# Kernel tuning notes

Measured on AMD Instinct MI355X. Metric: run time of the kernel, lower is better.

## Reference

```python
import jax, jax.numpy as jnp
import numpy as np

N = 2048      # feature_num (nodes/sensors)
T = 5         # timd_num (window length)
D = 64        # embed_dim
TOPK = 21     # topk + 1 (includes self, cos(i,i)=1)
B = 32        # batch
EPS = 1e-5
NEG_SLOPE = 0.2


def setup_inputs() -> dict:
    key = jax.random.key(0)
    ks = jax.random.split(key, 9)
    s = 1.0 / np.sqrt(D)
    return {
        "x": jax.random.normal(ks[0], (B, N, T), jnp.float32),
        "emb": jax.random.normal(ks[1], (N, D), jnp.float32) * s,      # embedding table
        "W": jax.random.normal(ks[2], (D, T), jnp.float32) * (1.0 / np.sqrt(T)),  # GNN lin weight
        "Wb": jax.random.normal(ks[3], (D,), jnp.float32) * 0.01,       # GNN lin bias
        "a_src": jax.random.normal(ks[4], (2 * D,), jnp.float32) * s,   # attention vec (source half)
        "a_dst": jax.random.normal(ks[5], (2 * D,), jnp.float32) * s,   # attention vec (dest half)
        "gamma": jnp.ones((D,), jnp.float32),                            # BatchNorm1d weight
        "beta": jnp.zeros((D,), jnp.float32),                            # BatchNorm1d bias
        "fc_w": jax.random.normal(ks[6], (1, D), jnp.float32) * s,      # fc weight
        "fc_b": jnp.zeros((1,), jnp.float32),                            # fc bias
    }


def reference(x, emb, W, Wb, a_src, a_dst, gamma, beta, fc_w, fc_b):
    # --- cosine-sim topk graph build ---
    norm = jnp.linalg.norm(emb, axis=-1)                    # [N]
    cos = (emb @ emb.T) / (norm[:, None] * norm[None, :])   # [N,N]
    _, idx = jax.lax.top_k(cos, TOPK)                       # [N,TOPK]
    # scatter one-hot adjacency (vectorized, no per-row loop)
    adj = jnp.zeros((N, N), x.dtype).at[jnp.arange(N)[:, None], idx].set(1.0)
    # --- GNN: GDN-style attention message passing ---
    h = jnp.einsum('bnt,dt->bnd', x, W) + Wb                # [B,N,D]
    g = jnp.concatenate([h, jnp.broadcast_to(emb, h.shape)], axis=-1)  # [B,N,2D]
    e_src = g @ a_src                                       # [B,N]
    e_dst = g @ a_dst                                       # [B,N]
    e = jax.nn.leaky_relu(e_src[:, :, None] + e_dst[:, None, :], NEG_SLOPE)  # [B,N,N]
    e = jnp.where(adj > 0, e, jnp.float32(-1e9))
    alpha = jax.nn.softmax(e, axis=-1)                      # [B,N,N], rows sum to 1 over TOPK nbrs
    z = jax.nn.relu(jnp.einsum('bij,bjd->bid', alpha, h))   # [B,N,D]
    # --- output head: z * emb, BN over channels, relu, fc ---
    out = z * emb                                           # [B,N,D]
    mean = out.mean(axis=(0, 1))                            # BN1d stats over (batch, nodes)
    var = out.var(axis=(0, 1))
    out = (out - mean) * jax.lax.rsqrt(var + EPS) * gamma + beta
    out = jax.nn.relu(out)
    out = out @ fc_w.T + fc_b                               # [B,N,1]
    return out.reshape(-1, N)                               # [B,N]
```

## Files before the change

### kernel.cpp

```cpp
#include <hip/hip_runtime.h>
#include <math.h>

#define N_NODES 2048
#define T_WIN 5
#define D_EMB 64
#define TOPK 21
#define B_BATCH 32
#define BN_TOTAL (B_BATCH * N_NODES)
#define EPS_BN 1e-5f
#define NEG_SLOPE 0.2f
#define STATS_STRIDE 16

typedef unsigned long long u64;

__device__ __forceinline__ float wave_sum(float v) {
#pragma unroll
    for (int off = 32; off > 0; off >>= 1) v += __shfl_xor(v, off, 64);
    return v;
}

__device__ __forceinline__ u64 max64(u64 a, u64 b) { return a > b ? a : b; }
__device__ __forceinline__ u64 min64(u64 a, u64 b) { return a < b ? a : b; }

__device__ __forceinline__ u64 bitonic_sort64_desc(u64 key, int lane) {
#pragma unroll
    for (int k = 2; k <= 64; k <<= 1) {
#pragma unroll
        for (int j = k >> 1; j >= 1; j >>= 1) {
            u64 pk = __shfl_xor(key, j, 64);
            bool dirDesc = ((lane & k) == 0);
            bool keepMax = (((lane & j) == 0) == dirDesc);
            key = keepMax ? max64(key, pk) : min64(key, pk);
        }
    }
    return key;
}

__device__ __forceinline__ u64 bitonic_merge_top64(u64 a, u64 b, int lane) {
    u64 br = __shfl(b, 63 - lane, 64);
    u64 c = max64(a, br);
#pragma unroll
    for (int j = 32; j >= 1; j >>= 1) {
        u64 pk = __shfl_xor(c, j, 64);
        bool keepMax = ((lane & j) == 0);
        c = keepMax ? max64(c, pk) : min64(c, pk);
    }
    return c;
}

__global__ __launch_bounds__(64) void k_node_pre(
    const float* __restrict__ emb, float* __restrict__ norms,
    float* __restrict__ stats, float* __restrict__ stats2) {
    int n = blockIdx.x;
    int d = threadIdx.x;
    if (n < 16) stats[n * 64 + d] = 0.f;
    else if (n < 32) stats2[(n - 16) * 64 + d] = 0.f;
    float e = emb[n * D_EMB + d];
    float s2 = wave_sum(e * e);
    if (d == 0) norms[n] = sqrtf(s2);
}

__global__ __launch_bounds__(256) void k_gram(
    const float* __restrict__ emb, const float* __restrict__ norms,
    float* __restrict__ cosM) {
    __shared__ __align__(16) float As[64][68];
    __shared__ __align__(16) float Bs[64][68];
    int t = threadIdx.x;
    int bi = blockIdx.x & 31, bj = blockIdx.x >> 5;
    int i0 = bi * 64, j0 = bj * 64;

    {
        int r = t >> 2, c0 = t & 3;
        const float4* srcA = (const float4*)(emb + (size_t)(i0 + r) * D_EMB);
        const float4* srcB = (const float4*)(emb + (size_t)(j0 + r) * D_EMB);
#pragma unroll
        for (int k = 0; k < 4; k++) {
            int f4 = c0 + 4 * k;
            float4 v = srcA[f4];
            int d = 4 * f4;
            As[d][r] = v.x; As[d + 1][r] = v.y; As[d + 2][r] = v.z; As[d + 3][r] = v.w;
            float4 w = srcB[f4];
            Bs[d][r] = w.x; Bs[d + 1][r] = w.y; Bs[d + 2][r] = w.z; Bs[d + 3][r] = w.w;
        }
    }
    __syncthreads();

    int ti = t & 15, tj = t >> 4;
    float acc[4][4] = {};
#pragma unroll
    for (int d = 0; d < 64; d++) {
        float4 a = *(const float4*)&As[d][4 * ti];
        float4 b = *(const float4*)&Bs[d][4 * tj];
        acc[0][0] += a.x * b.x; acc[0][1] += a.x * b.y; acc[0][2] += a.x * b.z; acc[0][3] += a.x * b.w;
        acc[1][0] += a.y * b.x; acc[1][1] += a.y * b.y; acc[1][2] += a.y * b.z; acc[1][3] += a.y * b.w;
        acc[2][0] += a.z * b.x; acc[2][1] += a.z * b.y; acc[2][2] += a.z * b.z; acc[2][3] += a.z * b.w;
        acc[3][0] += a.w * b.x; acc[3][1] += a.w * b.y; acc[3][2] += a.w * b.z; acc[3][3] += a.w * b.w;
    }

    float nis[4] = {norms[i0 + 4 * ti], norms[i0 + 4 * ti + 1],
                    norms[i0 + 4 * ti + 2], norms[i0 + 4 * ti + 3]};
    float njs[4] = {norms[j0 + 4 * tj], norms[j0 + 4 * tj + 1],
                    norms[j0 + 4 * tj + 2], norms[j0 + 4 * tj + 3]};
#pragma unroll
    for (int r = 0; r < 4; r++) {
        float4 o;
        o.x = acc[r][0] / (nis[r] * njs[0]);
        o.y = acc[r][1] / (nis[r] * njs[1]);
        o.z = acc[r][2] / (nis[r] * njs[2]);
        o.w = acc[r][3] / (nis[r] * njs[3]);
        *(float4*)(cosM + (size_t)(i0 + 4 * ti + r) * N_NODES + j0 + 4 * tj) = o;
    }
}

__global__ __launch_bounds__(256) void k_select(
    const float* __restrict__ cosM, int* __restrict__ idxT) {
    __shared__ u64 candbuf[4][128];
    int tid = threadIdx.x;
    int wid = tid >> 6, lane = tid & 63;
    int i = blockIdx.x * 4 + wid;
    const float* row = cosM + (size_t)i * N_NODES;
    u64* buf = candbuf[wid];

    u64 a = 0;
    u64 t = 0;
    int cnt = 0;
    float vcur = row[lane];

#pragma unroll 1
    for (int c = 0; c < N_NODES / 64; c++) {
        int j = c * 64 + lane;
        float v = vcur;
        if (c < N_NODES / 64 - 1) vcur = row[j + 64];
        unsigned u = __float_as_uint(v);
        u = (u & 0x80000000u) ? ~u : (u | 0x80000000u);
        u64 key = ((u64)u << 32) | (unsigned)(~j);
        unsigned long long ball = __ballot(key > t);
        if (ball) {
            int ofs = __popcll(ball & ((1ull << lane) - 1ull));
            if (key > t) buf[cnt + ofs] = key;
            cnt += (int)__popcll(ball);
            if (cnt >= 64) {
                u64 nk = buf[lane];
                nk = bitonic_sort64_desc(nk, lane);
                a = bitonic_merge_top64(a, nk, lane);
                t = __shfl(a, 20, 64);
                int rem = cnt - 64;
                u64 mv = (lane < rem) ? buf[64 + lane] : 0;
                if (lane < rem) buf[lane] = mv;
                cnt = rem;
            }
        }
    }
    while (cnt > 0) {
        int take = cnt < 64 ? cnt : 64;
        u64 nk = (lane < take) ? buf[lane] : 0;
        nk = bitonic_sort64_desc(nk, lane);
        a = bitonic_merge_top64(a, nk, lane);
        t = __shfl(a, 20, 64);
        int rem = cnt - take;
        u64 mv = (lane < rem) ? buf[take + lane] : 0;
        if (lane < rem) buf[lane] = mv;
        cnt = rem;
    }

    if (lane < TOPK) idxT[lane * N_NODES + i] = (int)(~(unsigned)a);
}

__global__ __launch_bounds__(256) void k_edge(
    const float* __restrict__ x, const float* __restrict__ W,
    const float* __restrict__ Wb, const float* __restrict__ a_src,
    const float* __restrict__ a_dst, const float* __restrict__ emb,
    float* __restrict__ es2T, float* __restrict__ ed2T) {
    int wid = threadIdx.x >> 6, lane = threadIdx.x & 63;
    int gw = blockIdx.x * 4 + wid;
    const float* wp = W + lane * T_WIN;
    float w0 = wp[0], w1 = wp[1], w2 = wp[2], w3 = wp[3], w4 = wp[4];
    float bias = Wb[lane];
    float as = a_src[lane], asE = a_src[D_EMB + lane];
    float ad = a_dst[lane], adE = a_dst[D_EMB + lane];

    for (int node = gw; node < BN_TOTAL; node += 8192) {
        int n = node & (N_NODES - 1);
        const float* xp = x + (size_t)node * T_WIN;
        float hv = bias + xp[0] * w0 + xp[1] * w1 + xp[2] * w2 + xp[3] * w3 + xp[4] * w4;
        float e = emb[n * D_EMB + lane];
        float es = wave_sum(hv * as + e * asE);
        float ed = wave_sum(hv * ad + e * adE);
        if (lane == 0) {
            es2T[node] = es;
            ed2T[node] = ed;
        }
    }
}

__global__ __launch_bounds__(256) void k_alpha(
    const int* __restrict__ idxT, const float* __restrict__ es2T,
    const float* __restrict__ ed2T, float* __restrict__ alphaT) {
    __shared__ float sed[N_NODES];
    int g = blockIdx.x;
    int b = g & 31;
    int i0 = (g >> 5) * 256;
    int t = threadIdx.x;

    {
        const float4* src = (const float4*)(ed2T + (size_t)b * N_NODES);
        float4* dst = (float4*)sed;
#pragma unroll
        for (int q = 0; q < 2; q++) dst[t + 256 * q] = src[t + 256 * q];
    }
    __syncthreads();

    int i = i0 + t;
    float es = es2T[(size_t)b * N_NODES + i];
    float ev[TOPK];
    float m = -3e38f;
#pragma unroll
    for (int k = 0; k < TOPK; k++) {
        int jk = idxT[k * N_NODES + i];
        float e = es + sed[jk];
        e = e > 0.f ? e : NEG_SLOPE * e;
        ev[k] = e;
        m = fmaxf(m, e);
    }
    float s = 0.f;
#pragma unroll
    for (int k = 0; k < TOPK; k++) {
        ev[k] = __expf(ev[k] - m);
        s += ev[k];
    }
    float inv = 1.0f / s;
#pragma unroll
    for (int k = 0; k < TOPK; k++)
        alphaT[((size_t)b * TOPK + k) * N_NODES + i] = ev[k] * inv;
}

__global__ __launch_bounds__(256, 4) void k_msg(
    const float* __restrict__ x, const float* __restrict__ W,
    const float* __restrict__ Wb, const int* __restrict__ idxT,
    const float* __restrict__ alphaT, const float* __restrict__ emb,
    float* __restrict__ obufT, float* __restrict__ stats,
    float* __restrict__ stats2) {
    __shared__ __align__(16) float hts[N_NODES][4];
    __shared__ float sred[2][4][4];

    int g = blockIdx.x;
    int b = (g & 7) + 8 * ((g >> 3) & 3);
    int rest = g >> 5;
    int c = rest & 15;
    int half = rest >> 4;
    int d0 = c * 4;
    int t = threadIdx.x;
    int wid = t >> 6, lane = t & 63;

    float wc[4][T_WIN], wb4[4];
#pragma unroll
    for (int q = 0; q < 4; q++) {
        wb4[q] = Wb[d0 + q];
#pragma unroll
        for (int tt = 0; tt < T_WIN; tt++) wc[q][tt] = W[(d0 + q) * T_WIN + tt];
    }
    const float* xb = x + (size_t)b * N_NODES * T_WIN;
#pragma unroll
    for (int r = 0; r < 8; r++) {
        int row = t + 256 * r;
        const float* xr = xb + row * T_WIN;
        float x0 = xr[0], x1 = xr[1], x2 = xr[2], x3 = xr[3], x4 = xr[4];
        float4 hv;
        hv.x = wb4[0] + x0 * wc[0][0] + x1 * wc[0][1] + x2 * wc[0][2] + x3 * wc[0][3] + x4 * wc[0][4];
        hv.y = wb4[1] + x0 * wc[1][0] + x1 * wc[1][1] + x2 * wc[1][2] + x3 * wc[1][3] + x4 * wc[1][4];
        hv.z = wb4[2] + x0 * wc[2][0] + x1 * wc[2][1] + x2 * wc[2][2] + x3 * wc[2][3] + x4 * wc[2][4];
        hv.w = wb4[3] + x0 * wc[3][0] + x1 * wc[3][1] + x2 * wc[3][2] + x3 * wc[3][3] + x4 * wc[3][4];
        *(float4*)&hts[row][0] = hv;
    }
    __syncthreads();

    float sacc[4] = {0.f, 0.f, 0.f, 0.f};
    float sacc2[4] = {0.f, 0.f, 0.f, 0.f};
    int ibase = half * 1024;
    const float* aT = alphaT + (size_t)b * TOPK * N_NODES;
#pragma unroll 1
    for (int r = 0; r < 4; r++) {
        int i = ibase + 256 * r + t;
        float4 z = make_float4(0.f, 0.f, 0.f, 0.f);
#pragma unroll
        for (int k = 0; k < TOPK; k++) {
            int jk = idxT[k * N_NODES + i];
            float a = aT[(size_t)k * N_NODES + i];
            float4 hv = *(const float4*)&hts[jk][0];
            z.x = fmaf(a, hv.x, z.x);
            z.y = fmaf(a, hv.y, z.y);
            z.z = fmaf(a, hv.z, z.z);
            z.w = fmaf(a, hv.w, z.w);
        }
        const float* ep = emb + (size_t)i * D_EMB + d0;
        float4 e4 = *(const float4*)ep;
        float4 o;
        o.x = fmaxf(z.x, 0.f) * e4.x;
        o.y = fmaxf(z.y, 0.f) * e4.y;
        o.z = fmaxf(z.z, 0.f) * e4.z;
        o.w = fmaxf(z.w, 0.f) * e4.w;
        ((float4*)obufT)[((size_t)c * B_BATCH + b) * N_NODES + i] = o;
        sacc[0] += o.x; sacc[1] += o.y; sacc[2] += o.z; sacc[3] += o.w;
        sacc2[0] += o.x * o.x; sacc2[1] += o.y * o.y;
        sacc2[2] += o.z * o.z; sacc2[3] += o.w * o.w;
    }

#pragma unroll
    for (int q = 0; q < 4; q++) {
        sacc[q] = wave_sum(sacc[q]);
        sacc2[q] = wave_sum(sacc2[q]);
    }
    if (lane == 0) {
#pragma unroll
        for (int q = 0; q < 4; q++) {
            sred[0][wid][q] = sacc[q];
            sred[1][wid][q] = sacc2[q];
        }
    }
    __syncthreads();
    if (t < 8) {
        int q = t & 3, which = t >> 2;
        float v = sred[which][0][q] + sred[which][1][q] + sred[which][2][q] + sred[which][3][q];
        float* dst = which ? stats2 : stats;
        atomicAdd(&dst[(d0 + q) * STATS_STRIDE], v);
    }
}

__global__ __launch_bounds__(256) void k_out(
    const float* __restrict__ obufT, const float* __restrict__ stats,
    const float* __restrict__ stats2, const float* __restrict__ gamma,
    const float* __restrict__ beta, const float* __restrict__ fc_w,
    const float* __restrict__ fc_b, float* __restrict__ out) {
    int t = threadIdx.x;
    int wid = t >> 6, lane = t & 63;
    int nloc = lane >> 4, c = lane & 15;
    const float invM = 1.0f / (float)BN_TOTAL;

    float mean[4], inv[4], g4[4], bt4[4], fw4[4];
#pragma unroll
    for (int q = 0; q < 4; q++) {
        int d = 4 * c + q;
        float mn = stats[d * STATS_STRIDE] * invM;
        float var = stats2[d * STATS_STRIDE] * invM - mn * mn;
        mean[q] = mn;
        inv[q] = rsqrtf(var + EPS_BN);
        g4[q] = gamma[d]; bt4[q] = beta[d]; fw4[q] = fc_w[d];
    }
    float fb = fc_b[0];

#pragma unroll 1
    for (int r = 0; r < 16; r++) {
        int nd = blockIdx.x * 256 + r * 16 + wid * 4 + nloc;
        int b = nd >> 11, n = nd & (N_NODES - 1);
        float4 o = ((const float4*)obufT)[((size_t)c * B_BATCH + b) * N_NODES + n];
        float p = 0.f;
        float v;
        v = fmaxf((o.x - mean[0]) * inv[0] * g4[0] + bt4[0], 0.f); p = fmaf(v, fw4[0], p);
        v = fmaxf((o.y - mean[1]) * inv[1] * g4[1] + bt4[1], 0.f); p = fmaf(v, fw4[1], p);
        v = fmaxf((o.z - mean[2]) * inv[2] * g4[2] + bt4[2], 0.f); p = fmaf(v, fw4[2], p);
        v = fmaxf((o.w - mean[3]) * inv[3] * g4[3] + bt4[3], 0.f); p = fmaf(v, fw4[3], p);
#pragma unroll
        for (int off = 1; off <= 8; off <<= 1) p += __shfl_xor(p, off, 64);
        if (c == 0) out[nd] = p + fb;
    }
}

extern "C" void kernel_launch(void* const* d_in, const int* in_sizes, int n_in,
                              void* d_out, int out_size, void* d_ws, size_t ws_size,
                              hipStream_t stream) {
    const float* x     = (const float*)d_in[0];
    const float* emb   = (const float*)d_in[1];
    const float* W     = (const float*)d_in[2];
    const float* Wb    = (const float*)d_in[3];
    const float* a_src = (const float*)d_in[4];
    const float* a_dst = (const float*)d_in[5];
    const float* gamma = (const float*)d_in[6];
    const float* beta  = (const float*)d_in[7];
    const float* fc_w  = (const float*)d_in[8];
    const float* fc_b  = (const float*)d_in[9];
    float* out = (float*)d_out;

    char* ws = (char*)d_ws;
    float* stats  = (float*)(ws + 0);
    float* stats2 = (float*)(ws + 4096);
    int*   idxT   = (int*)  (ws + 8192);
    float* norms  = (float*)(ws + 180224);
    float* es2T   = (float*)(ws + 188416);
    float* ed2T   = (float*)(ws + 450560);
    float* alphaT = (float*)(ws + 712704);
    float* cosM   = (float*)(ws + 6217728);
    float* obufT  = cosM;

    k_node_pre<<<N_NODES, 64, 0, stream>>>(emb, norms, stats, stats2);
    k_gram<<<1024, 256, 0, stream>>>(emb, norms, cosM);
    k_select<<<N_NODES / 4, 256, 0, stream>>>(cosM, idxT);
    k_edge<<<2048, 256, 0, stream>>>(x, W, Wb, a_src, a_dst, emb, es2T, ed2T);
    k_alpha<<<256, 256, 0, stream>>>(idxT, es2T, ed2T, alphaT);
    k_msg<<<1024, 256, 0, stream>>>(x, W, Wb, idxT, alphaT, emb, obufT, stats, stats2);
    k_out<<<256, 256, 0, stream>>>(obufT, stats, stats2, gamma, beta, fc_w, fc_b, out);
}
```

Baseline: 156.1 us.

## Exploit cosine symmetry in gram, fuse norm pre-pass into edge kernel, retile msg

Computes only lower-triangular 64x64 tiles of the cosine matrix and mirrors each result into the transposed position, roughly halving gram FLOPs and launches. Folds the norm computation and stats zeroing into k_edge to remove a launch. Reworks k_msg so each block covers all nodes with a padded stride-6 shared layout and float2 loads, and halves k_out per-block work. The mirrored writes are scattered scalar stores, which adds uncoalesced traffic.

```diff
diff --git a/kernel.cpp b/kernel.cpp
--- a/kernel.cpp
+++ b/kernel.cpp
@@ -48,16 +48,41 @@
     return c;
 }
 
-__global__ __launch_bounds__(64) void k_node_pre(
-    const float* __restrict__ emb, float* __restrict__ norms,
-    float* __restrict__ stats, float* __restrict__ stats2) {
-    int n = blockIdx.x;
-    int d = threadIdx.x;
-    if (n < 16) stats[n * 64 + d] = 0.f;
-    else if (n < 32) stats2[(n - 16) * 64 + d] = 0.f;
-    float e = emb[n * D_EMB + d];
-    float s2 = wave_sum(e * e);
-    if (d == 0) norms[n] = sqrtf(s2);
+__global__ __launch_bounds__(256) void k_edge(
+    const float* __restrict__ x, const float* __restrict__ W,
+    const float* __restrict__ Wb, const float* __restrict__ a_src,
+    const float* __restrict__ a_dst, const float* __restrict__ emb,
+    float* __restrict__ es2T, float* __restrict__ ed2T,
+    float* __restrict__ norms, float* __restrict__ stats,
+    float* __restrict__ stats2) {
+    if (blockIdx.x < 2) {
+        float* p = blockIdx.x ? stats2 : stats;
+        ((float4*)p)[threadIdx.x] = make_float4(0.f, 0.f, 0.f, 0.f);
+    }
+    int wid = threadIdx.x >> 6, lane = threadIdx.x & 63;
+    int gw = blockIdx.x * 4 + wid;
+    const float* wp = W + lane * T_WIN;
+    float w0 = wp[0], w1 = wp[1], w2 = wp[2], w3 = wp[3], w4 = wp[4];
+    float bias = Wb[lane];
+    float as = a_src[lane], asE = a_src[D_EMB + lane];
+    float ad = a_dst[lane], adE = a_dst[D_EMB + lane];
+
+    for (int node = gw; node < BN_TOTAL; node += 8192) {
+        int n = node & (N_NODES - 1);
+        const float* xp = x + (size_t)node * T_WIN;
+        float hv = bias + xp[0] * w0 + xp[1] * w1 + xp[2] * w2 + xp[3] * w3 + xp[4] * w4;
+        float e = emb[n * D_EMB + lane];
+        if (node < N_NODES) {
+            float s2 = wave_sum(e * e);
+            if (lane == 0) norms[node] = sqrtf(s2);
+        }
+        float es = wave_sum(hv * as + e * asE);
+        float ed = wave_sum(hv * ad + e * adE);
+        if (lane == 0) {
+            es2T[node] = es;
+            ed2T[node] = ed;
+        }
+    }
 }
 
 __global__ __launch_bounds__(256) void k_gram(
@@ -66,8 +91,12 @@
     __shared__ __align__(16) float As[64][68];
     __shared__ __align__(16) float Bs[64][68];
     int t = threadIdx.x;
-    int bi = blockIdx.x & 31, bj = blockIdx.x >> 5;
-    int i0 = bi * 64, j0 = bj * 64;
+    int g = blockIdx.x;
+    int a = (int)((sqrtf(8.f * g + 1.f) - 1.f) * 0.5f);
+    while ((a + 1) * (a + 2) / 2 <= g) a++;
+    while (a * (a + 1) / 2 > g) a--;
+    int bq = g - a * (a + 1) / 2;
+    int i0 = a * 64, j0 = bq * 64;
 
     {
         int r = t >> 2, c0 = t & 3;
@@ -89,12 +118,12 @@
     float acc[4][4] = {};
 #pragma unroll
     for (int d = 0; d < 64; d++) {
-        float4 a = *(const float4*)&As[d][4 * ti];
-        float4 b = *(const float4*)&Bs[d][4 * tj];
-        acc[0][0] += a.x * b.x; acc[0][1] += a.x * b.y; acc[0][2] += a.x * b.z; acc[0][3] += a.x * b.w;
-        acc[1][0] += a.y * b.x; acc[1][1] += a.y * b.y; acc[1][2] += a.y * b.z; acc[1][3] += a.y * b.w;
-        acc[2][0] += a.z * b.x; acc[2][1] += a.z * b.y; acc[2][2] += a.z * b.z; acc[2][3] += a.z * b.w;
-        acc[3][0] += a.w * b.x; acc[3][1] += a.w * b.y; acc[3][2] += a.w * b.z; acc[3][3] += a.w * b.w;
+        float4 av = *(const float4*)&As[d][4 * ti];
+        float4 bv = *(const float4*)&Bs[d][4 * tj];
+        acc[0][0] += av.x * bv.x; acc[0][1] += av.x * bv.y; acc[0][2] += av.x * bv.z; acc[0][3] += av.x * bv.w;
+        acc[1][0] += av.y * bv.x; acc[1][1] += av.y * bv.y; acc[1][2] += av.y * bv.z; acc[1][3] += av.y * bv.w;
+        acc[2][0] += av.z * bv.x; acc[2][1] += av.z * bv.y; acc[2][2] += av.z * bv.z; acc[2][3] += av.z * bv.w;
+        acc[3][0] += av.w * bv.x; acc[3][1] += av.w * bv.y; acc[3][2] += av.w * bv.z; acc[3][3] += av.w * bv.w;
     }
 
     float nis[4] = {norms[i0 + 4 * ti], norms[i0 + 4 * ti + 1],
@@ -108,7 +137,12 @@
         o.y = acc[r][1] / (nis[r] * njs[1]);
         o.z = acc[r][2] / (nis[r] * njs[2]);
         o.w = acc[r][3] / (nis[r] * njs[3]);
-        *(float4*)(cosM + (size_t)(i0 + 4 * ti + r) * N_NODES + j0 + 4 * tj) = o;
+        int i = i0 + 4 * ti + r;
+        *(float4*)(cosM + (size_t)i * N_NODES + j0 + 4 * tj) = o;
+        cosM[(size_t)(j0 + 4 * tj + 0) * N_NODES + i] = o.x;
+        cosM[(size_t)(j0 + 4 * tj + 1) * N_NODES + i] = o.y;
+        cosM[(size_t)(j0 + 4 * tj + 2) * N_NODES + i] = o.z;
+        cosM[(size_t)(j0 + 4 * tj + 3) * N_NODES + i] = o.w;
     }
 }
 
@@ -166,33 +200,6 @@
     if (lane < TOPK) idxT[lane * N_NODES + i] = (int)(~(unsigned)a);
 }
 
-__global__ __launch_bounds__(256) void k_edge(
-    const float* __restrict__ x, const float* __restrict__ W,
-    const float* __restrict__ Wb, const float* __restrict__ a_src,
-    const float* __restrict__ a_dst, const float* __restrict__ emb,
-    float* __restrict__ es2T, float* __restrict__ ed2T) {
-    int wid = threadIdx.x >> 6, lane = threadIdx.x & 63;
-    int gw = blockIdx.x * 4 + wid;
-    const float* wp = W + lane * T_WIN;
-    float w0 = wp[0], w1 = wp[1], w2 = wp[2], w3 = wp[3], w4 = wp[4];
-    float bias = Wb[lane];
-    float as = a_src[lane], asE = a_src[D_EMB + lane];
-    float ad = a_dst[lane], adE = a_dst[D_EMB + lane];
-
-    for (int node = gw; node < BN_TOTAL; node += 8192) {
-        int n = node & (N_NODES - 1);
-        const float* xp = x + (size_t)node * T_WIN;
-        float hv = bias + xp[0] * w0 + xp[1] * w1 + xp[2] * w2 + xp[3] * w3 + xp[4] * w4;
-        float e = emb[n * D_EMB + lane];
-        float es = wave_sum(hv * as + e * asE);
-        float ed = wave_sum(hv * ad + e * adE);
-        if (lane == 0) {
-            es2T[node] = es;
-            ed2T[node] = ed;
-        }
-    }
-}
-
 __global__ __launch_bounds__(256) void k_alpha(
     const int* __restrict__ idxT, const float* __restrict__ es2T,
     const float* __restrict__ ed2T, float* __restrict__ alphaT) {
@@ -234,20 +241,18 @@
         alphaT[((size_t)b * TOPK + k) * N_NODES + i] = ev[k] * inv;
 }
 
-__global__ __launch_bounds__(256, 4) void k_msg(
+__global__ __launch_bounds__(256, 2) void k_msg(
     const float* __restrict__ x, const float* __restrict__ W,
     const float* __restrict__ Wb, const int* __restrict__ idxT,
     const float* __restrict__ alphaT, const float* __restrict__ emb,
     float* __restrict__ obufT, float* __restrict__ stats,
     float* __restrict__ stats2) {
-    __shared__ __align__(16) float hts[N_NODES][4];
+    __shared__ float hts[N_NODES][6];
     __shared__ float sred[2][4][4];
 
     int g = blockIdx.x;
     int b = (g & 7) + 8 * ((g >> 3) & 3);
-    int rest = g >> 5;
-    int c = rest & 15;
-    int half = rest >> 4;
+    int c = g >> 5;
     int d0 = c * 4;
     int t = threadIdx.x;
     int wid = t >> 6, lane = t & 63;
@@ -265,35 +270,34 @@
         int row = t + 256 * r;
         const float* xr = xb + row * T_WIN;
         float x0 = xr[0], x1 = xr[1], x2 = xr[2], x3 = xr[3], x4 = xr[4];
-        float4 hv;
-        hv.x = wb4[0] + x0 * wc[0][0] + x1 * wc[0][1] + x2 * wc[0][2] + x3 * wc[0][3] + x4 * wc[0][4];
-        hv.y = wb4[1] + x0 * wc[1][0] + x1 * wc[1][1] + x2 * wc[1][2] + x3 * wc[1][3] + x4 * wc[1][4];
-        hv.z = wb4[2] + x0 * wc[2][0] + x1 * wc[2][1] + x2 * wc[2][2] + x3 * wc[2][3] + x4 * wc[2][4];
-        hv.w = wb4[3] + x0 * wc[3][0] + x1 * wc[3][1] + x2 * wc[3][2] + x3 * wc[3][3] + x4 * wc[3][4];
-        *(float4*)&hts[row][0] = hv;
+        float h0 = wb4[0] + x0 * wc[0][0] + x1 * wc[0][1] + x2 * wc[0][2] + x3 * wc[0][3] + x4 * wc[0][4];
+        float h1 = wb4[1] + x0 * wc[1][0] + x1 * wc[1][1] + x2 * wc[1][2] + x3 * wc[1][3] + x4 * wc[1][4];
+        float h2 = wb4[2] + x0 * wc[2][0] + x1 * wc[2][1] + x2 * wc[2][2] + x3 * wc[2][3] + x4 * wc[2][4];
+        float h3 = wb4[3] + x0 * wc[3][0] + x1 * wc[3][1] + x2 * wc[3][2] + x3 * wc[3][3] + x4 * wc[3][4];
+        *(float2*)&hts[row][0] = make_float2(h0, h1);
+        *(float2*)&hts[row][2] = make_float2(h2, h3);
     }
     __syncthreads();
 
     float sacc[4] = {0.f, 0.f, 0.f, 0.f};
     float sacc2[4] = {0.f, 0.f, 0.f, 0.f};
-    int ibase = half * 1024;
     const float* aT = alphaT + (size_t)b * TOPK * N_NODES;
 #pragma unroll 1
-    for (int r = 0; r < 4; r++) {
-        int i = ibase + 256 * r + t;
+    for (int r = 0; r < 8; r++) {
+        int i = 256 * r + t;
         float4 z = make_float4(0.f, 0.f, 0.f, 0.f);
 #pragma unroll
         for (int k = 0; k < TOPK; k++) {
             int jk = idxT[k * N_NODES + i];
             float a = aT[(size_t)k * N_NODES + i];
-            float4 hv = *(const float4*)&hts[jk][0];
-            z.x = fmaf(a, hv.x, z.x);
-            z.y = fmaf(a, hv.y, z.y);
-            z.z = fmaf(a, hv.z, z.z);
-            z.w = fmaf(a, hv.w, z.w);
-        }
-        const float* ep = emb + (size_t)i * D_EMB + d0;
-        float4 e4 = *(const float4*)ep;
+            float2 h01 = *(const float2*)&hts[jk][0];
+            float2 h23 = *(const float2*)&hts[jk][2];
+            z.x = fmaf(a, h01.x, z.x);
+            z.y = fmaf(a, h01.y, z.y);
+            z.z = fmaf(a, h23.x, z.z);
+            z.w = fmaf(a, h23.y, z.w);
+        }
+        float4 e4 = *(const float4*)(emb + (size_t)i * D_EMB + d0);
         float4 o;
         o.x = fmaxf(z.x, 0.f) * e4.x;
         o.y = fmaxf(z.y, 0.f) * e4.y;
@@ -349,8 +353,8 @@
     float fb = fc_b[0];
 
 #pragma unroll 1
-    for (int r = 0; r < 16; r++) {
-        int nd = blockIdx.x * 256 + r * 16 + wid * 4 + nloc;
+    for (int r = 0; r < 8; r++) {
+        int nd = blockIdx.x * 128 + r * 16 + wid * 4 + nloc;
         int b = nd >> 11, n = nd & (N_NODES - 1);
         float4 o = ((const float4*)obufT)[((size_t)c * B_BATCH + b) * N_NODES + n];
         float p = 0.f;
@@ -391,11 +395,11 @@
     float* cosM   = (float*)(ws + 6217728);
     float* obufT  = cosM;
 
-    k_node_pre<<<N_NODES, 64, 0, stream>>>(emb, norms, stats, stats2);
-    k_gram<<<1024, 256, 0, stream>>>(emb, norms, cosM);
+    k_edge<<<2048, 256, 0, stream>>>(x, W, Wb, a_src, a_dst, emb,
+                                     es2T, ed2T, norms, stats, stats2);
+    k_gram<<<528, 256, 0, stream>>>(emb, norms, cosM);
     k_select<<<N_NODES / 4, 256, 0, stream>>>(cosM, idxT);
-    k_edge<<<2048, 256, 0, stream>>>(x, W, Wb, a_src, a_dst, emb, es2T, ed2T);
     k_alpha<<<256, 256, 0, stream>>>(idxT, es2T, ed2T, alphaT);
-    k_msg<<<1024, 256, 0, stream>>>(x, W, Wb, idxT, alphaT, emb, obufT, stats, stats2);
-    k_out<<<256, 256, 0, stream>>>(obufT, stats, stats2, gamma, beta, fc_w, fc_b, out);
-}
+    k_msg<<<512, 256, 0, stream>>>(x, W, Wb, idxT, alphaT, emb, obufT, stats, stats2);
+    k_out<<<512, 256, 0, stream>>>(obufT, stats, stats2, gamma, beta, fc_w, fc_b, out);
+}
```

New measurement: 152.1 us. -2.5%, faster.
